# Kernel optimization log

Hardware: AMD Instinct MI355X
Metric: run time of the kernel (lower is better)

The kernel has to match this reference:

```python
import jax, jax.numpy as jnp
import numpy as np

E = 8          # num_experts
K = 2          # top_k
CAPF = 1.25    # capacity_factor


def setup_inputs() -> dict:
    key = jax.random.key(0)
    ks = jax.random.split(key, 6)
    B, T, C = 4, 2048, 1024
    x = jax.random.normal(ks[0], (B, T, C), jnp.float32)
    noise = jax.random.normal(ks[1], (B, T, E), jnp.float32)  # stands in for torch.randn_like
    Wr = jax.random.normal(ks[2], (C, E), jnp.float32) * 0.02   # topkroute_linear
    Wn = jax.random.normal(ks[3], (C, E), jnp.float32) * 0.02   # noise_linear
    W1 = jax.random.normal(ks[4], (E, C, 4 * C), jnp.float32) * 0.02  # expert up-proj
    W2 = jax.random.normal(ks[5], (E, 4 * C, C), jnp.float32) * 0.02  # expert down-proj
    return {"x": x, "noise": noise, "Wr": Wr, "Wn": Wn, "W1": W1, "W2": W2}


def reference(x, noise, Wr, Wn, W1, W2):
    B, T, C = x.shape
    N = B * T
    cap = int(N * K / E * CAPF)  # expert_capacity (static)

    # --- NoisyTopkRouter ---
    logits = x @ Wr                                  # [B,T,E]
    noise_logits = x @ Wn                            # [B,T,E]
    noisy = logits + noise * jax.nn.softplus(noise_logits)
    _, idx = jax.lax.top_k(noisy, K)                 # [B,T,K]
    mask_bte = (idx[..., None] == jnp.arange(E)).any(axis=-2)       # [B,T,E]
    gating = jax.nn.softmax(jnp.where(mask_bte, noisy, -jnp.inf), axis=-1)

    flat_x = x.reshape(N, C)
    flat_g = gating.reshape(N, E)

    # --- capacity-limited dispatch (token order, first `cap` per expert) ---
    mask = mask_bte.reshape(N, E).T                  # [E,N]
    rank = jnp.cumsum(mask, axis=1) - 1              # position within expert
    keep = mask & (rank < cap)
    slot = jnp.where(keep, rank, cap)                # overflow -> dump slot `cap`
    tok = jnp.where(keep, jnp.arange(N)[None, :], N) # dropped -> pad token `N`
    s2t = jnp.full((E, cap + 1), N, dtype=jnp.int32)
    s2t = s2t.at[jnp.arange(E)[:, None], slot].set(tok.astype(jnp.int32))[:, :cap]  # [E,cap]

    # --- gather, grouped GEMM (Linear-SiLU-Linear), weight, scatter-add ---
    x_pad = jnp.concatenate([flat_x, jnp.zeros((1, C), flat_x.dtype)], axis=0)
    xin = x_pad[s2t]                                 # [E,cap,C]
    h = jax.nn.silu(jnp.einsum('enc,ech->enh', xin, W1))
    out = jnp.einsum('enh,ehc->enc', h, W2)          # [E,cap,C]
    g_pad = jnp.concatenate([flat_g, jnp.zeros((1, E), flat_g.dtype)], axis=0)
    gate = g_pad[s2t, jnp.arange(E)[:, None]]        # [E,cap]
    weighted = out * gate[..., None]
    upd = jnp.zeros((N + 1, C), x.dtype).at[s2t.reshape(-1)].add(weighted.reshape(-1, C))
    return upd[:N].reshape(B, T, C)
```

## Files before the change

kernel.cpp:

```cpp
#include <hip/hip_runtime.h>
#include <hip/hip_bf16.h>
#include <math.h>

#define C_DIM 1024
#define H_DIM 4096
#define E_NUM 8

typedef __bf16 bf16x8 __attribute__((ext_vector_type(8)));
typedef float f32x4 __attribute__((ext_vector_type(4)));
typedef unsigned u32x4 __attribute__((ext_vector_type(4)));

__device__ __forceinline__ unsigned short f2bf(float f) {
  union { float f; unsigned u; } v; v.f = f;
  unsigned r = v.u + 0x7FFFu + ((v.u >> 16) & 1u);
  return (unsigned short)(r >> 16);
}

__device__ __forceinline__ void gload16(const short* g, short* l) {
  __builtin_amdgcn_global_load_lds(
      (const __attribute__((address_space(1))) unsigned int*)g,
      (__attribute__((address_space(3))) unsigned int*)l, 16, 0, 0);
}

__device__ __forceinline__ f32x4 mfma16(u32x4 a, u32x4 b, f32x4 c) {
  return __builtin_amdgcn_mfma_f32_16x16x32_bf16(
      __builtin_bit_cast(bf16x8, a), __builtin_bit_cast(bf16x8, b), c, 0, 0, 0);
}

#define DSR(v, a, imm) asm volatile("ds_read_b128 %0, %1 offset:" #imm : "=v"(v) : "v"(a))
#define LGKM0 { asm volatile("s_waitcnt lgkmcnt(0)" ::: "memory"); __builtin_amdgcn_sched_barrier(0); }
#define VMW(n) asm volatile("s_waitcnt vmcnt(" #n ")" ::: "memory")
#define LDS_U32(p) ((unsigned)(size_t)(__attribute__((address_space(3))) short*)(p))

__global__ __launch_bounds__(256) void router_kernel(
    const float* __restrict__ x, const float* __restrict__ noise,
    const float* __restrict__ Wr, const float* __restrict__ Wn,
    int2* __restrict__ idx_out, float2* __restrict__ gate_out, int N)
{
  int t = blockIdx.x;
  int tid = threadIdx.x;
  const float* xrow = x + (size_t)t * C_DIM;
  float accR[E_NUM], accN[E_NUM];
#pragma unroll
  for (int e = 0; e < E_NUM; e++) { accR[e] = 0.f; accN[e] = 0.f; }
  for (int c = tid; c < C_DIM; c += 256) {
    float xv = xrow[c];
    const float* wr = Wr + (size_t)c * E_NUM;
    const float* wn = Wn + (size_t)c * E_NUM;
#pragma unroll
    for (int e = 0; e < E_NUM; e++) {
      accR[e] = fmaf(xv, wr[e], accR[e]);
      accN[e] = fmaf(xv, wn[e], accN[e]);
    }
  }
#pragma unroll
  for (int e = 0; e < E_NUM; e++) {
    for (int off = 32; off > 0; off >>= 1) {
      accR[e] += __shfl_down(accR[e], off, 64);
      accN[e] += __shfl_down(accN[e], off, 64);
    }
  }
  __shared__ float red[4][2 * E_NUM];
  int lane = tid & 63, wave = tid >> 6;
  if (lane == 0) {
#pragma unroll
    for (int e = 0; e < E_NUM; e++) { red[wave][e] = accR[e]; red[wave][E_NUM + e] = accN[e]; }
  }
  __syncthreads();
  if (tid == 0) {
    float ns[E_NUM];
#pragma unroll
    for (int e = 0; e < E_NUM; e++) {
      float lg = red[0][e] + red[1][e] + red[2][e] + red[3][e];
      float nl = red[0][E_NUM + e] + red[1][E_NUM + e] + red[2][E_NUM + e] + red[3][E_NUM + e];
      float sp = fmaxf(nl, 0.f) + log1pf(expf(-fabsf(nl)));
      ns[e] = lg + noise[(size_t)t * E_NUM + e] * sp;
    }
    int i1 = 0; float m1 = ns[0];
    int i2 = -1; float m2 = -INFINITY;
#pragma unroll
    for (int e = 1; e < E_NUM; e++) {
      float v = ns[e];
      if (v > m1) { m2 = m1; i2 = i1; m1 = v; i1 = e; }
      else if (v > m2) { m2 = v; i2 = e; }
    }
    float e2 = expf(m2 - m1);
    float s = 1.f + e2;
    gate_out[t] = make_float2(1.f / s, e2 / s);
    idx_out[t] = make_int2(i1, i2);
  }
}

__global__ __launch_bounds__(256) void scan_kernel(
    const int2* __restrict__ idx, const float2* __restrict__ gates,
    int* __restrict__ s2t, float* __restrict__ gslot, int* __restrict__ counts,
    int N, int cap)
{
  int e = blockIdx.x;
  int tid = threadIdx.x;
  for (int s = tid; s < cap; s += 256) { s2t[(size_t)e * cap + s] = N; gslot[(size_t)e * cap + s] = 0.f; }
  __syncthreads();
  __shared__ int wtot[4];
  int lane = tid & 63, wave = tid >> 6;
  int running = 0;
  for (int base = 0; base < N; base += 256) {
    int t = base + tid;
    int2 ix = idx[t];
    bool flag = (ix.x == e) || (ix.y == e);
    unsigned long long m = __ballot(flag);
    int rank = __popcll(m & ((1ull << lane) - 1ull));
    if (lane == 0) wtot[wave] = __popcll(m);
    __syncthreads();
    int woff = 0;
    for (int w = 0; w < wave; w++) woff += wtot[w];
    int slot = running + woff + rank;
    if (flag && slot < cap) {
      s2t[(size_t)e * cap + slot] = t;
      gslot[(size_t)e * cap + slot] = (ix.x == e) ? gates[t].x : gates[t].y;
    }
    running += wtot[0] + wtot[1] + wtot[2] + wtot[3];
    __syncthreads();
  }
  if (tid == 0) counts[e] = min(running, cap);
}

__global__ __launch_bounds__(256) void convert_x_kernel(
    const float* __restrict__ src, short* __restrict__ dst, int n8)
{
  int i = blockIdx.x * 256 + threadIdx.x;
  if (i >= n8) return;
  const float4* s = (const float4*)src + (size_t)i * 2;
  float4 a = s[0], b = s[1];
  union { unsigned short us[8]; uint4 v; } o;
  o.us[0] = f2bf(a.x); o.us[1] = f2bf(a.y); o.us[2] = f2bf(a.z); o.us[3] = f2bf(a.w);
  o.us[4] = f2bf(b.x); o.us[5] = f2bf(b.y); o.us[6] = f2bf(b.z); o.us[7] = f2bf(b.w);
  ((uint4*)dst)[i] = o.v;
}

__global__ __launch_bounds__(256) void transpose_convert_kernel(
    const float* __restrict__ src, short* __restrict__ dst,
    int R, int Cc)
{
  src += (size_t)blockIdx.z * R * Cc;
  dst += (size_t)blockIdx.z * (size_t)R * Cc;
  __shared__ float tile[64][65];
  int c0 = blockIdx.x * 64, r0 = blockIdx.y * 64;
  int tid = threadIdx.x;
  int tr = tid >> 4, tc = (tid & 15) * 4;
#pragma unroll
  for (int p = 0; p < 4; p++) {
    int r = p * 16 + tr;
    float4 v = *(const float4*)(src + (size_t)(r0 + r) * Cc + c0 + tc);
    tile[r][tc] = v.x; tile[r][tc + 1] = v.y; tile[r][tc + 2] = v.z; tile[r][tc + 3] = v.w;
  }
  __syncthreads();
#pragma unroll
  for (int p = 0; p < 4; p++) {
    int c = p * 16 + tr;
    union { unsigned short us[4]; ushort4 v; } o;
#pragma unroll
    for (int j = 0; j < 4; j++) o.us[j] = f2bf(tile[tc + j][c]);
    *(ushort4*)(dst + (size_t)(c0 + c) * R + r0 + tc) = o.v;
  }
}

template<int MODE>
__global__ __launch_bounds__(512, 2) void gemm_moe(
    const short* __restrict__ Abase, const short* __restrict__ Wt,
    const int* __restrict__ s2t, const float* __restrict__ gslot,
    const int* __restrict__ counts, void* __restrict__ outp,
    int cap, int N, int rows)
{
  __shared__ short As[3][8192];
  __shared__ short Bs[3][8192];

  int flat = blockIdx.x;
  int e = flat & 7;
  int s = flat >> 3;
  int r = s % rows;
  int t = s / rows;
  int c, kc;
  if (MODE == 0) { c = t; kc = 0; }
  else           { c = t & 3; kc = t >> 2; }

  int cnt = counts[e];
  int row0 = r * 256;
  if (row0 >= cnt) return;
  int col0 = c * 256;

  int tid = threadIdx.x;
  int w = tid >> 6, l = tid & 63;
  int wr = w >> 2, wc = w & 3;
  int rowT = tid & 255, kbT = tid >> 8;

  const int NS = 32;

  const short *pA, *pB;
  if (MODE == 0) {
    int tok = min(s2t[(size_t)e * cap + row0 + rowT], N - 1);
    pA = Abase + (size_t)tok * C_DIM;
    pB = Wt + (size_t)e * (C_DIM * H_DIM) + (size_t)(col0 + rowT) * C_DIM;
  } else {
    pA = Abase + ((size_t)e * cap + row0 + rowT) * H_DIM + kc * 1024;
    pB = Wt + (size_t)e * (C_DIM * H_DIM) + (size_t)(col0 + rowT) * H_DIM + kc * 1024;
  }

  unsigned aB = LDS_U32(As) + (unsigned)((l >> 4) * 4096 + (wr * 128 + (l & 15)) * 16);
  unsigned bB = LDS_U32(Bs) + (unsigned)((l >> 4) * 4096 + (wc * 64 + (l & 15)) * 16);

  f32x4 acc[8][4];
#pragma unroll
  for (int m = 0; m < 8; m++)
#pragma unroll
    for (int n = 0; n < 4; n++) acc[m][n] = 0.f;

#define STAGE(k0, buf) { \
  gload16(pA + (k0) + kbT * 8,       &As[buf][kbT * 2048 + rowT * 8]); \
  gload16(pA + (k0) + (kbT + 2) * 8, &As[buf][(kbT + 2) * 2048 + rowT * 8]); \
  gload16(pB + (k0) + kbT * 8,       &Bs[buf][kbT * 2048 + rowT * 8]); \
  gload16(pB + (k0) + (kbT + 2) * 8, &Bs[buf][(kbT + 2) * 2048 + rowT * 8]); }

  STAGE(0, 0);
  STAGE(32, 1);

  unsigned bufR = 0;
  int bufS = 2;
#pragma unroll 1
  for (int i = 0; i < NS; ++i) {
    if (i == NS - 1) { VMW(0); } else { VMW(4); }
    __builtin_amdgcn_s_barrier();
    __builtin_amdgcn_sched_barrier(0);

    u32x4 af[8], bg[4];
    unsigned aA = aB + bufR, bA = bB + bufR;
    DSR(af[0], aA, 0);    DSR(af[1], aA, 256);  DSR(af[2], aA, 512);  DSR(af[3], aA, 768);
    DSR(af[4], aA, 1024); DSR(af[5], aA, 1280); DSR(af[6], aA, 1536); DSR(af[7], aA, 1792);
    DSR(bg[0], bA, 0);    DSR(bg[1], bA, 256);  DSR(bg[2], bA, 512);  DSR(bg[3], bA, 768);

    if (i + 2 < NS) {
      STAGE((i + 2) * 32, bufS);
      bufS = (bufS == 2) ? 0 : bufS + 1;
    }

    LGKM0;
    __builtin_amdgcn_s_setprio(1);
#pragma unroll
    for (int m = 0; m < 8; m++)
#pragma unroll
      for (int n = 0; n < 4; n++)
        acc[m][n] = mfma16(af[m], bg[n], acc[m][n]);
    __builtin_amdgcn_s_setprio(0);

    bufR = (bufR == 32768u) ? 0u : bufR + 16384u;
  }
#undef STAGE

  int orow = row0 + wr * 128 + (l >> 4) * 4;
  int ocol = col0 + wc * 64 + (l & 15);
  if (MODE == 0) {
    short* hE = (short*)outp + (size_t)e * cap * H_DIM;
#pragma unroll
    for (int m = 0; m < 8; m++)
#pragma unroll
      for (int rr = 0; rr < 4; rr++) {
        int slot = orow + m * 16 + rr;
        float g = gslot[(size_t)e * cap + slot];
        size_t rb = (size_t)slot * H_DIM + ocol;
#pragma unroll
        for (int n = 0; n < 4; n++) {
          float v = acc[m][n][rr];
          hE[rb + n * 16] = (short)f2bf(g * (v / (1.f + expf(-v))));
        }
      }
  } else {
    float* out = (float*)outp;
#pragma unroll
    for (int m = 0; m < 8; m++)
#pragma unroll
      for (int rr = 0; rr < 4; rr++) {
        int slot = orow + m * 16 + rr;
        int tok = s2t[(size_t)e * cap + slot];
        if (tok < N) {
          float* op = out + (size_t)tok * C_DIM + ocol;
#pragma unroll
          for (int n = 0; n < 4; n++)
            atomicAdd(op + n * 16, acc[m][n][rr]);
        }
      }
  }
}

extern "C" void kernel_launch(void* const* d_in, const int* in_sizes, int n_in,
                              void* d_out, int out_size, void* d_ws, size_t ws_size,
                              hipStream_t stream)
{
  const float* x     = (const float*)d_in[0];
  const float* noise = (const float*)d_in[1];
  const float* Wr    = (const float*)d_in[2];
  const float* Wn    = (const float*)d_in[3];
  const float* W1    = (const float*)d_in[4];
  const float* W2    = (const float*)d_in[5];
  float* out = (float*)d_out;

  int N = in_sizes[0] / C_DIM;
  int cap = (int)((double)N * 2.0 / E_NUM * 1.25);
  int rows = cap / 256;

  size_t off = 0;
  auto alloc = [&](size_t bytes) -> char* {
    char* r = (char*)d_ws + off;
    off += (bytes + 255) & ~(size_t)255;
    return r;
  };
  int2*   idx    = (int2*)alloc((size_t)N * sizeof(int2));
  float2* gates  = (float2*)alloc((size_t)N * sizeof(float2));
  int*    s2t    = (int*)alloc((size_t)E_NUM * cap * sizeof(int));
  float*  gslot  = (float*)alloc((size_t)E_NUM * cap * sizeof(float));
  int*    counts = (int*)alloc(E_NUM * sizeof(int));
  short*  xbf    = (short*)alloc((size_t)N * C_DIM * sizeof(short));
  short*  W1t    = (short*)alloc((size_t)E_NUM * C_DIM * H_DIM * sizeof(short));
  short*  W2t    = (short*)alloc((size_t)E_NUM * C_DIM * H_DIM * sizeof(short));
  short*  h      = (short*)alloc((size_t)E_NUM * cap * H_DIM * sizeof(short));
  (void)ws_size;

  hipMemsetAsync(d_out, 0, (size_t)out_size * sizeof(float), stream);
  router_kernel<<<N, 256, 0, stream>>>(x, noise, Wr, Wn, idx, gates, N);
  scan_kernel<<<E_NUM, 256, 0, stream>>>(idx, gates, s2t, gslot, counts, N, cap);
  convert_x_kernel<<<(N * C_DIM / 8 + 255) / 256, 256, 0, stream>>>(x, xbf, N * C_DIM / 8);
  transpose_convert_kernel<<<dim3(H_DIM / 64, C_DIM / 64, E_NUM), 256, 0, stream>>>(
      W1, W1t, C_DIM, H_DIM);
  transpose_convert_kernel<<<dim3(C_DIM / 64, H_DIM / 64, E_NUM), 256, 0, stream>>>(
      W2, W2t, H_DIM, C_DIM);

  gemm_moe<0><<<dim3(E_NUM * rows * (H_DIM / 256)), 512, 0, stream>>>(
      xbf, W1t, s2t, gslot, counts, h, cap, N, rows);
  gemm_moe<1><<<dim3(E_NUM * rows * 4 * 4), 512, 0, stream>>>(
      h, W2t, s2t, gslot, counts, out, cap, N, rows);
}
```

Before: 810.4 us.

## Switch MoE GEMM to 32x32x16 MFMA with 4-wave 128x128 warp tiles

```diff
diff --git a/kernel.cpp b/kernel.cpp
--- a/kernel.cpp
+++ b/kernel.cpp
@@ -8,6 +8,7 @@
 
 typedef __bf16 bf16x8 __attribute__((ext_vector_type(8)));
 typedef float f32x4 __attribute__((ext_vector_type(4)));
+typedef float f32x16 __attribute__((ext_vector_type(16)));
 typedef unsigned u32x4 __attribute__((ext_vector_type(4)));
 
 __device__ __forceinline__ unsigned short f2bf(float f) {
@@ -22,8 +23,8 @@
       (__attribute__((address_space(3))) unsigned int*)l, 16, 0, 0);
 }
 
-__device__ __forceinline__ f32x4 mfma16(u32x4 a, u32x4 b, f32x4 c) {
-  return __builtin_amdgcn_mfma_f32_16x16x32_bf16(
+__device__ __forceinline__ f32x16 mfma32(u32x4 a, u32x4 b, f32x16 c) {
+  return __builtin_amdgcn_mfma_f32_32x32x16_bf16(
       __builtin_bit_cast(bf16x8, a), __builtin_bit_cast(bf16x8, b), c, 0, 0, 0);
 }
 
@@ -165,7 +166,7 @@
 }
 
 template<int MODE>
-__global__ __launch_bounds__(512, 2) void gemm_moe(
+__global__ __launch_bounds__(256, 1) void gemm_moe(
     const short* __restrict__ Abase, const short* __restrict__ Wt,
     const int* __restrict__ s2t, const float* __restrict__ gslot,
     const int* __restrict__ counts, void* __restrict__ outp,
@@ -190,35 +191,38 @@
 
   int tid = threadIdx.x;
   int w = tid >> 6, l = tid & 63;
-  int wr = w >> 2, wc = w & 3;
-  int rowT = tid & 255, kbT = tid >> 8;
+  int wr = w >> 1, wc = w & 1;
 
   const int NS = 32;
 
   const short *pA, *pB;
   if (MODE == 0) {
-    int tok = min(s2t[(size_t)e * cap + row0 + rowT], N - 1);
+    int tok = min(s2t[(size_t)e * cap + row0 + tid], N - 1);
     pA = Abase + (size_t)tok * C_DIM;
-    pB = Wt + (size_t)e * (C_DIM * H_DIM) + (size_t)(col0 + rowT) * C_DIM;
+    pB = Wt + (size_t)e * (C_DIM * H_DIM) + (size_t)(col0 + tid) * C_DIM;
   } else {
-    pA = Abase + ((size_t)e * cap + row0 + rowT) * H_DIM + kc * 1024;
-    pB = Wt + (size_t)e * (C_DIM * H_DIM) + (size_t)(col0 + rowT) * H_DIM + kc * 1024;
-  }
-
-  unsigned aB = LDS_U32(As) + (unsigned)((l >> 4) * 4096 + (wr * 128 + (l & 15)) * 16);
-  unsigned bB = LDS_U32(Bs) + (unsigned)((l >> 4) * 4096 + (wc * 64 + (l & 15)) * 16);
-
-  f32x4 acc[8][4];
-#pragma unroll
-  for (int m = 0; m < 8; m++)
-#pragma unroll
-    for (int n = 0; n < 4; n++) acc[m][n] = 0.f;
+    pA = Abase + ((size_t)e * cap + row0 + tid) * H_DIM + kc * 1024;
+    pB = Wt + (size_t)e * (C_DIM * H_DIM) + (size_t)(col0 + tid) * H_DIM + kc * 1024;
+  }
+
+  unsigned aB = LDS_U32(As) + (unsigned)((l >> 5) * 4096 + (wr * 128 + (l & 31)) * 16);
+  unsigned bB = LDS_U32(Bs) + (unsigned)((l >> 5) * 4096 + (wc * 128 + (l & 31)) * 16);
+
+  f32x16 acc[4][4];
+#pragma unroll
+  for (int ti = 0; ti < 4; ti++)
+#pragma unroll
+    for (int tj = 0; tj < 4; tj++) acc[ti][tj] = 0.f;
 
 #define STAGE(k0, buf) { \
-  gload16(pA + (k0) + kbT * 8,       &As[buf][kbT * 2048 + rowT * 8]); \
-  gload16(pA + (k0) + (kbT + 2) * 8, &As[buf][(kbT + 2) * 2048 + rowT * 8]); \
-  gload16(pB + (k0) + kbT * 8,       &Bs[buf][kbT * 2048 + rowT * 8]); \
-  gload16(pB + (k0) + (kbT + 2) * 8, &Bs[buf][(kbT + 2) * 2048 + rowT * 8]); }
+  gload16(pA + (k0),      &As[buf][tid * 8]); \
+  gload16(pA + (k0) + 8,  &As[buf][2048 + tid * 8]); \
+  gload16(pA + (k0) + 16, &As[buf][4096 + tid * 8]); \
+  gload16(pA + (k0) + 24, &As[buf][6144 + tid * 8]); \
+  gload16(pB + (k0),      &Bs[buf][tid * 8]); \
+  gload16(pB + (k0) + 8,  &Bs[buf][2048 + tid * 8]); \
+  gload16(pB + (k0) + 16, &Bs[buf][4096 + tid * 8]); \
+  gload16(pB + (k0) + 24, &Bs[buf][6144 + tid * 8]); }
 
   STAGE(0, 0);
   STAGE(32, 1);
@@ -227,15 +231,16 @@
   int bufS = 2;
 #pragma unroll 1
   for (int i = 0; i < NS; ++i) {
-    if (i == NS - 1) { VMW(0); } else { VMW(4); }
+    if (i == NS - 1) { VMW(0); } else { VMW(8); }
     __builtin_amdgcn_s_barrier();
     __builtin_amdgcn_sched_barrier(0);
 
-    u32x4 af[8], bg[4];
+    u32x4 af[2][4], bg[2][4];
     unsigned aA = aB + bufR, bA = bB + bufR;
-    DSR(af[0], aA, 0);    DSR(af[1], aA, 256);  DSR(af[2], aA, 512);  DSR(af[3], aA, 768);
-    DSR(af[4], aA, 1024); DSR(af[5], aA, 1280); DSR(af[6], aA, 1536); DSR(af[7], aA, 1792);
-    DSR(bg[0], bA, 0);    DSR(bg[1], bA, 256);  DSR(bg[2], bA, 512);  DSR(bg[3], bA, 768);
+    DSR(af[0][0], aA, 0);    DSR(af[0][1], aA, 512);  DSR(af[0][2], aA, 1024); DSR(af[0][3], aA, 1536);
+    DSR(af[1][0], aA, 8192); DSR(af[1][1], aA, 8704); DSR(af[1][2], aA, 9216); DSR(af[1][3], aA, 9728);
+    DSR(bg[0][0], bA, 0);    DSR(bg[0][1], bA, 512);  DSR(bg[0][2], bA, 1024); DSR(bg[0][3], bA, 1536);
+    DSR(bg[1][0], bA, 8192); DSR(bg[1][1], bA, 8704); DSR(bg[1][2], bA, 9216); DSR(bg[1][3], bA, 9728);
 
     if (i + 2 < NS) {
       STAGE((i + 2) * 32, bufS);
@@ -245,46 +250,49 @@
     LGKM0;
     __builtin_amdgcn_s_setprio(1);
 #pragma unroll
-    for (int m = 0; m < 8; m++)
-#pragma unroll
-      for (int n = 0; n < 4; n++)
-        acc[m][n] = mfma16(af[m], bg[n], acc[m][n]);
+    for (int p = 0; p < 2; p++)
+#pragma unroll
+      for (int ti = 0; ti < 4; ti++)
+#pragma unroll
+        for (int tj = 0; tj < 4; tj++)
+          acc[ti][tj] = mfma32(af[p][ti], bg[p][tj], acc[ti][tj]);
     __builtin_amdgcn_s_setprio(0);
 
     bufR = (bufR == 32768u) ? 0u : bufR + 16384u;
   }
 #undef STAGE
 
-  int orow = row0 + wr * 128 + (l >> 4) * 4;
-  int ocol = col0 + wc * 64 + (l & 15);
+  int rbase = row0 + wr * 128;
+  int cbase = col0 + wc * 128 + (l & 31);
+  int rlane = 4 * (l >> 5);
   if (MODE == 0) {
     short* hE = (short*)outp + (size_t)e * cap * H_DIM;
 #pragma unroll
-    for (int m = 0; m < 8; m++)
-#pragma unroll
-      for (int rr = 0; rr < 4; rr++) {
-        int slot = orow + m * 16 + rr;
+    for (int ti = 0; ti < 4; ti++)
+#pragma unroll
+      for (int rr = 0; rr < 16; rr++) {
+        int slot = rbase + ti * 32 + (rr & 3) + 8 * (rr >> 2) + rlane;
         float g = gslot[(size_t)e * cap + slot];
-        size_t rb = (size_t)slot * H_DIM + ocol;
-#pragma unroll
-        for (int n = 0; n < 4; n++) {
-          float v = acc[m][n][rr];
-          hE[rb + n * 16] = (short)f2bf(g * (v / (1.f + expf(-v))));
+        size_t rb = (size_t)slot * H_DIM + cbase;
+#pragma unroll
+        for (int tj = 0; tj < 4; tj++) {
+          float v = acc[ti][tj][rr];
+          hE[rb + tj * 32] = (short)f2bf(g * (v / (1.f + expf(-v))));
         }
       }
   } else {
     float* out = (float*)outp;
 #pragma unroll
-    for (int m = 0; m < 8; m++)
-#pragma unroll
-      for (int rr = 0; rr < 4; rr++) {
-        int slot = orow + m * 16 + rr;
+    for (int ti = 0; ti < 4; ti++)
+#pragma unroll
+      for (int rr = 0; rr < 16; rr++) {
+        int slot = rbase + ti * 32 + (rr & 3) + 8 * (rr >> 2) + rlane;
         int tok = s2t[(size_t)e * cap + slot];
         if (tok < N) {
-          float* op = out + (size_t)tok * C_DIM + ocol;
-#pragma unroll
-          for (int n = 0; n < 4; n++)
-            atomicAdd(op + n * 16, acc[m][n][rr]);
+          float* op = out + (size_t)tok * C_DIM + cbase;
+#pragma unroll
+          for (int tj = 0; tj < 4; tj++)
+            atomicAdd(op + tj * 32, acc[ti][tj][rr]);
         }
       }
   }
@@ -332,8 +340,8 @@
   transpose_convert_kernel<<<dim3(C_DIM / 64, H_DIM / 64, E_NUM), 256, 0, stream>>>(
       W2, W2t, H_DIM, C_DIM);
 
-  gemm_moe<0><<<dim3(E_NUM * rows * (H_DIM / 256)), 512, 0, stream>>>(
+  gemm_moe<0><<<dim3(E_NUM * rows * (H_DIM / 256)), 256, 0, stream>>>(
       xbf, W1t, s2t, gslot, counts, h, cap, N, rows);
-  gemm_moe<1><<<dim3(E_NUM * rows * 4 * 4), 512, 0, stream>>>(
+  gemm_moe<1><<<dim3(E_NUM * rows * 4 * 4), 256, 0, stream>>>(
       h, W2t, s2t, gslot, counts, out, cap, N, rows);
 }
```

Result: slower. 915.7 us (+13.0%).
